# Optimization experiments

Measured on AMD Instinct MI355X. Metric: run time of the kernel, lower is better.

## Reference

```python
import jax, jax.numpy as jnp
import numpy as np

B, T = 8, 1024
C, H, K, FF, L = 512, 8, 64, 2048, 6
STATE, INP, NBINS, NACT, MAXT = 128, 128, 41, 16, 2048
EPS = 1e-5


def _ln(x, g, b):
    m = jnp.mean(x, axis=-1, keepdims=True)
    v = jnp.var(x, axis=-1, keepdims=True)
    return (x - m) / jnp.sqrt(v + EPS) * g + b


def setup_inputs() -> dict:
    key = jax.random.key(0)
    ks = jax.random.split(key, 24)
    s = 0.02
    d = {}
    d["obs"] = jax.random.normal(ks[0], (B, T, STATE), jnp.float32)
    d["action"] = jax.random.randint(ks[1], (B, T), 0, NACT)
    d["step"] = jax.random.randint(ks[2], (B, T), 0, MAXT)
    # embeddings / input projections
    d["W_obs"] = s * jax.random.normal(ks[3], (STATE, C), jnp.float32)
    d["b_obs"] = jnp.zeros((C,), jnp.float32)
    d["E_act"] = s * jax.random.normal(ks[4], (NACT, C), jnp.float32)
    d["W_traj"] = s * jax.random.normal(ks[5], (2 * C, C), jnp.float32)
    d["b_traj"] = jnp.zeros((C,), jnp.float32)
    d["E_time"] = s * jax.random.normal(ks[6], (MAXT, C), jnp.float32)
    # per-layer stacked params (scanned over leading L axis)
    d["Wq"] = s * jax.random.normal(ks[7], (L, H, C, K), jnp.float32)
    d["Wk"] = s * jax.random.normal(ks[8], (L, H, C, K), jnp.float32)
    d["Wv"] = s * jax.random.normal(ks[9], (L, H, C, K), jnp.float32)
    d["Wp"] = s * jax.random.normal(ks[10], (L, H * K, C), jnp.float32)
    d["bp"] = jnp.zeros((L, C), jnp.float32)
    d["W1"] = s * jax.random.normal(ks[11], (L, C, FF), jnp.float32)
    d["b1"] = jnp.zeros((L, FF), jnp.float32)
    d["W2"] = s * jax.random.normal(ks[12], (L, FF, C), jnp.float32)
    d["b2"] = jnp.zeros((L, C), jnp.float32)
    d["g1"] = jnp.ones((L, C), jnp.float32)
    d["be1"] = jnp.zeros((L, C), jnp.float32)
    d["g2"] = jnp.ones((L, C), jnp.float32)
    d["be2"] = jnp.zeros((L, C), jnp.float32)
    # final norm + heads
    d["gf"] = jnp.ones((C,), jnp.float32)
    d["bf"] = jnp.zeros((C,), jnp.float32)
    d["W_oh"] = s * jax.random.normal(ks[13], (C, INP), jnp.float32)
    d["b_oh"] = jnp.zeros((INP,), jnp.float32)
    d["W_rh"] = s * jax.random.normal(ks[14], (C, NBINS), jnp.float32)
    d["b_rh"] = jnp.zeros((NBINS,), jnp.float32)
    d["W_dh"] = s * jax.random.normal(ks[15], (C, 1), jnp.float32)
    d["b_dh"] = jnp.zeros((1,), jnp.float32)
    return d


def reference(obs, action, step, W_obs, b_obs, E_act, W_traj, b_traj, E_time,
              Wq, Wk, Wv, Wp, bp, W1, b1, W2, b2, g1, be1, g2, be2,
              gf, bf, W_oh, b_oh, W_rh, b_rh, W_dh, b_dh):
    Bc, Tc = obs.shape[0], obs.shape[1]
    obs_emb = obs @ W_obs + b_obs                      # [B,T,C]
    act_emb = E_act[action]                            # [B,T,C]
    token = jnp.concatenate([obs_emb, act_emb], -1) @ W_traj + b_traj
    x = token + E_time[step]                           # [B,T,C]

    causal = jnp.tril(jnp.ones((Tc, Tc), bool))        # [T,T]
    scale = 1.0 / jnp.sqrt(jnp.asarray(K, x.dtype))

    def block(x, p):
        wq, wk, wv, wp, bpl, w1, b1l, w2, b2l, ga, ba, gb, bb = p
        q = jnp.einsum('btc,hck->bhtk', x, wq)
        k = jnp.einsum('btc,hck->bhtk', x, wk)
        v = jnp.einsum('btc,hck->bhtk', x, wv)
        wei = jnp.einsum('bhtk,bhsk->bhts', q, k) * scale
        wei = jnp.where(causal, wei, -jnp.inf)
        att = jax.nn.softmax(wei, axis=-1)             # dropout off (eval)
        o = jnp.einsum('bhts,bhsk->bhtk', att, v)
        o = o.transpose(0, 2, 1, 3).reshape(Bc, Tc, H * K)  # head-wise concat
        y = o @ wp + bpl
        x = _ln(x + y, ga, ba)                         # post-norm, as in source
        y = jax.nn.relu(x @ w1 + b1l) @ w2 + b2l
        x = _ln(x + y, gb, bb)
        return x, None

    x, _ = jax.lax.scan(block, x, (Wq, Wk, Wv, Wp, bp, W1, b1, W2, b2, g1, be1, g2, be2))
    x = _ln(x, gf, bf)
    obs_logits = x @ W_oh + b_oh
    reward_logits = x @ W_rh + b_rh
    done_logits = x @ W_dh + b_dh
    return (obs_logits, reward_logits, done_logits)
```

## Files before the change

kernel.cpp:

```cpp
#include <hip/hip_runtime.h>
#include <hip/hip_bf16.h>


#define TSEQ 1024
#define BB   8
#define CDIM 512
#define HH   8
#define KHD  64
#define FFD  2048
#define LL   6
#define MROWS (BB*TSEQ)

typedef __hip_bfloat16 bf16;
typedef __attribute__((ext_vector_type(8))) short bf16x8;
typedef __attribute__((ext_vector_type(4))) short bf16x4;
typedef __attribute__((ext_vector_type(4))) float f32x4;

#define MFMA16K16(a,b,c) __builtin_amdgcn_mfma_f32_16x16x16bf16_1k(a,b,c,0,0,0)

static __device__ __forceinline__ short f2bf_bits(float x) {
    bf16 t = __float2bfloat16(x);
    return *reinterpret_cast<short*>(&t);
}
static __device__ __forceinline__ float bf2f(short b) {
    unsigned u = ((unsigned)(unsigned short)b) << 16;
    return __uint_as_float(u);
}

static __device__ __forceinline__ void gload_lds16(const bf16* g, short* l) {
    __builtin_amdgcn_global_load_lds(
        (__attribute__((address_space(1))) const void*)g,
        (__attribute__((address_space(3))) void*)l, 16, 0, 0);
}

struct PrepJob { const float* src; long dstOff; int nrows; int kd; int type; };
struct PrepArgs { PrepJob jobs[48]; };

__global__ void __launch_bounds__(256) prep_weights(PrepArgs args, bf16* __restrict__ wsb)
{
    PrepJob J = args.jobs[blockIdx.y];
    const int tilesK = (J.kd + 63) >> 6;
    const int tilesN = (J.nrows + 63) >> 6;
    const int t = blockIdx.x;
    if (t >= tilesK * tilesN) return;
    const int tn = t / tilesK, tk = t - tn * tilesK;
    const int n0 = tn << 6, k0 = tk << 6;

    __shared__ float tile[64][65];
    const int tid = threadIdx.x;
    const bool full = (J.type != 3) && (n0 + 64 <= J.nrows) && (k0 + 64 <= J.kd);

    if (full) {
        const int c4 = (tid & 15) * 4;
        const int r0 = tid >> 4;
#pragma unroll
        for (int i = 0; i < 4; ++i) {
            int kl = r0 + i * 16;
            int k = k0 + kl;
            const float* src;
            if (J.type == 0) src = J.src + (long)k * J.nrows + n0 + c4;
            else             src = J.src + ((long)(n0 >> 6) * J.kd + k) * 64 + c4;
            float4 v = *(const float4*)src;
            tile[kl][c4 + 0] = v.x; tile[kl][c4 + 1] = v.y;
            tile[kl][c4 + 2] = v.z; tile[kl][c4 + 3] = v.w;
        }
        __syncthreads();
        const int kq = (tid & 15) * 4;
        const int n1 = tid >> 4;
#pragma unroll
        for (int i = 0; i < 4; ++i) {
            int nl = n1 + i * 16;
            bf16x4 o;
#pragma unroll
            for (int j2 = 0; j2 < 4; ++j2) o[j2] = f2bf_bits(tile[kq + j2][nl]);
            *(bf16x4*)(wsb + J.dstOff + (long)(n0 + nl) * J.kd + k0 + kq) = o;
        }
    } else {
#pragma unroll
        for (int i = 0; i < 16; ++i) {
            int e = tid + i * 256;
            int kl = e >> 6, nl = e & 63;
            int k = k0 + kl, n = n0 + nl;
            float v = 0.f;
            if (J.type != 3 && k < J.kd && n < J.nrows) {
                if (J.type == 0) v = J.src[(long)k * J.nrows + n];
                else             v = J.src[((long)(n >> 6) * J.kd + k) * 64 + (n & 63)];
            }
            tile[kl][nl] = v;
        }
        __syncthreads();
#pragma unroll
        for (int i = 0; i < 16; ++i) {
            int e = tid + i * 256;
            int nl = e >> 6, kl = e & 63;
            int n = n0 + nl, k = k0 + kl;
            if (n < J.nrows && k < J.kd)
                wsb[J.dstOff + (long)n * J.kd + k] = __float2bfloat16(tile[kl][nl]);
        }
    }
}

__global__ void build_head_bias(const float* __restrict__ b_oh, const float* __restrict__ b_rh,
                                const float* __restrict__ b_dh, float* __restrict__ hb)
{
    int i = threadIdx.x;
    float v = 0.f;
    if (i < 128) v = b_oh[i];
    else if (i < 169) v = b_rh[i - 128];
    else if (i == 169) v = b_dh[0];
    hb[i] = v;
}

template<int TN, int BK, int OUTMODE, bool BIAS, bool RELU>
__global__ void __launch_bounds__(256) gemm_kernel(
    const bf16* __restrict__ A, const bf16* __restrict__ BT,
    void* __restrict__ Cout, const float* __restrict__ bias,
    int M, int N, int Kd,
    const void* __restrict__ aux1, const float* __restrict__ aux2)
{
    constexpr int NJ = TN / 32;
    constexpr int SL = BK / 8;
    constexpr int AI = (128 * BK) / (8 * 256);
    constexpr int BI = (TN  * BK) / (8 * 256);
    __shared__ short As[128 * BK];
    __shared__ short Bs[TN * BK];
    const int tid = threadIdx.x;
    const int lane = tid & 63;
    const int w = tid >> 6;
    const int wm = w >> 1, wn = w & 1;
    const int m0 = blockIdx.x * 128;
    const int n0 = blockIdx.y * TN;
    const int g = lane >> 4, lr = lane & 15;

    f32x4 acc[4][NJ] = {};

    for (int k0 = 0; k0 < Kd; k0 += BK) {
#pragma unroll
        for (int it = 0; it < AI; ++it) {
            int cbase = (w * AI + it) * 64;
            int c = cbase + lane;
            int row = c / SL, slot = c % SL;
            int ss = slot ^ (row & (SL - 1));
            gload_lds16(A + (size_t)(m0 + row) * Kd + k0 + ss * 8, As + cbase * 8);
        }
#pragma unroll
        for (int it = 0; it < BI; ++it) {
            int cbase = (w * BI + it) * 64;
            int c = cbase + lane;
            int row = c / SL, slot = c % SL;
            int ss = slot ^ (row & (SL - 1));
            gload_lds16(BT + (size_t)(n0 + row) * Kd + k0 + ss * 8, Bs + cbase * 8);
        }
        __syncthreads();
#pragma unroll
        for (int kk = 0; kk < BK; kk += 32) {
            bf16x8 af[4], bfr[NJ];
#pragma unroll
            for (int i = 0; i < 4; ++i) {
                int row = wm*64 + i*16 + lr;
                int ss = ((kk >> 3) + g) ^ (row & (SL - 1));
                af[i] = *(const bf16x8*)(As + row * BK + ss * 8);
            }
#pragma unroll
            for (int j = 0; j < NJ; ++j) {
                int row = wn*(TN/2) + j*16 + lr;
                int ss = ((kk >> 3) + g) ^ (row & (SL - 1));
                bfr[j] = *(const bf16x8*)(Bs + row * BK + ss * 8);
            }
#pragma unroll
            for (int i = 0; i < 4; ++i)
#pragma unroll
                for (int j = 0; j < NJ; ++j)
                    acc[i][j] = __builtin_amdgcn_mfma_f32_16x16x32_bf16(af[i], bfr[j], acc[i][j], 0, 0, 0);
        }
        __syncthreads();
    }

#pragma unroll
    for (int i = 0; i < 4; ++i) {
#pragma unroll
        for (int j = 0; j < NJ; ++j) {
            int col = n0 + wn*(TN/2) + j*16 + lr;
            float bv = 0.f;
            if (BIAS) bv = bias[col];
#pragma unroll
            for (int r = 0; r < 4; ++r) {
                int row = m0 + wm*64 + i*16 + g*4 + r;
                float v = acc[i][j][r] + bv;
                if (RELU) v = fmaxf(v, 0.f);
                if (OUTMODE == 1) {
                    ((bf16*)Cout)[(size_t)row * N + col] = __float2bfloat16(v);
                } else if (OUTMODE == 2) {
                    float* outf = (float*)Cout;
                    if (col < 128)      outf[(size_t)row * 128 + col] = v;
                    else if (col < 169) outf[1048576 + (size_t)row * 41 + (col - 128)] = v;
                    else if (col == 169) outf[1384448 + (size_t)row] = v;
                } else if (OUTMODE == 4) {
                    const int* stp = (const int*)aux1;
                    v += aux2[(size_t)stp[row] * 512 + col];
                    ((bf16*)Cout)[(size_t)row * N + col] = __float2bfloat16(v);
                } else {
                    ((float*)Cout)[(size_t)row * N + col] = v;
                }
            }
        }
    }
}

__global__ void __launch_bounds__(256) attn_kernel(const bf16* __restrict__ qkv, bf16* __restrict__ o)
{
    const int bh = blockIdx.x;
    const int z  = blockIdx.y;
    const int b = bh >> 3, h = bh & 7;
    const int tid = threadIdx.x, lane = tid & 63, w = tid >> 6;
    const int g = lane >> 4, lr = lane & 15;
    const int qlo = z, qhi = 15 - z;
    const float SCL = 0.125f * 1.44269504089f;

    __shared__ short Ks[128][72];
    __shared__ short Vs[8192];

    const size_t base = (size_t)b * TSEQ * 1536;

    bf16x8 qfL[2], qfH[2];
#pragma unroll
    for (int kk = 0; kk < 2; ++kk) {
        qfL[kk] = *(const bf16x8*)(qkv + base + (size_t)(qlo*64 + w*16 + lr) * 1536 + h*64 + kk*32 + g*8);
        qfH[kk] = *(const bf16x8*)(qkv + base + (size_t)(qhi*64 + w*16 + lr) * 1536 + h*64 + kk*32 + g*8);
    }

    f32x4 accL[4] = {}, accH[4] = {};
    float mL = -1e30f, lL = 0.f, mH = -1e30f, lH = 0.f;

    const short* vtr = &Vs[lane * 4];

    auto proc = [&](const bf16x8* qf, f32x4* acc, float& m, float& l, int qt, int kt) {
        f32x4 st[8];
        __builtin_amdgcn_s_setprio(1);
#pragma unroll
        for (int j = 0; j < 8; ++j) {
            st[j] = f32x4{0.f, 0.f, 0.f, 0.f};
#pragma unroll
            for (int kk = 0; kk < 2; ++kk) {
                bf16x8 af = *(const bf16x8*)(&Ks[j*16 + lr][kk*32 + g*8]);
                st[j] = __builtin_amdgcn_mfma_f32_16x16x32_bf16(af, qf[kk], st[j], 0, 0, 0);
            }
        }
        __builtin_amdgcn_s_setprio(0);
        const int qg = qt*64 + w*16 + lr;
        const bool diag = (kt == (qt >> 1));
        float vmax = -1e30f;
#pragma unroll
        for (int j = 0; j < 8; ++j)
#pragma unroll
            for (int r = 0; r < 4; ++r) {
                float v = st[j][r] * SCL;
                if (diag && (kt*128 + j*16 + g*4 + r) > qg) v = -1e30f;
                st[j][r] = v;
                vmax = fmaxf(vmax, v);
            }
        vmax = fmaxf(vmax, __shfl_xor(vmax, 16));
        vmax = fmaxf(vmax, __shfl_xor(vmax, 32));
        if (!__all(vmax <= m + 8.f)) {
            float mn = fmaxf(m, vmax);
            float alpha = exp2f(m - mn);
            l *= alpha;
            float av[4];
#pragma unroll
            for (int r = 0; r < 4; ++r) av[r] = __shfl(alpha, g*4 + r);
#pragma unroll
            for (int dj = 0; dj < 4; ++dj)
#pragma unroll
                for (int r = 0; r < 4; ++r) acc[dj][r] *= av[r];
            m = mn;
        }
        float psum = 0.f;
        bf16x4 pf[8];
#pragma unroll
        for (int j = 0; j < 8; ++j)
#pragma unroll
            for (int r = 0; r < 4; ++r) {
                float p = exp2f(st[j][r] - m);
                psum += p;
                pf[j][r] = f2bf_bits(p);
            }
        psum += __shfl_xor(psum, 16);
        psum += __shfl_xor(psum, 32);
        l += psum;
#pragma unroll
        for (int half = 0; half < 4; ++half) {
            bf16x4 vf[2][4];
#pragma unroll
            for (int jj = 0; jj < 2; ++jj)
#pragma unroll
                for (int dj = 0; dj < 4; ++dj) {
                    asm volatile("ds_read_b64_tr_b16 %0, %1"
                        : "=v"(vf[jj][dj])
                        : "v"((const __attribute__((address_space(3))) short*)
                              (vtr + ((half*2 + jj)*4 + dj) * 256)));
                }
            asm volatile("s_waitcnt lgkmcnt(0)" ::: "memory");
            __builtin_amdgcn_sched_barrier(0);
            __builtin_amdgcn_s_setprio(1);
#pragma unroll
            for (int jj = 0; jj < 2; ++jj)
#pragma unroll
                for (int dj = 0; dj < 4; ++dj)
                    acc[dj] = MFMA16K16(pf[half*2 + jj], vf[jj][dj], acc[dj]);
            __builtin_amdgcn_s_setprio(0);
        }
    };

    const int ktmax = qhi >> 1;
    for (int kt = 0; kt <= ktmax; ++kt) {
#pragma unroll
        for (int it = 0; it < 4; ++it) {
            int idx = tid + it * 256;
            int row = idx >> 3;
            int col = (idx & 7) << 3;
            *(bf16x8*)(&Ks[row][col]) =
                *(const bf16x8*)(qkv + base + (size_t)(kt*128 + row)*1536 + 512 + h*64 + col);
            bf16x8 vv = *(const bf16x8*)(qkv + base + (size_t)(kt*128 + row)*1536 + 1024 + h*64 + col);
            int dst = ((row >> 4)*4 + (col >> 4))*256 + (row & 15)*16 + (col & 8);
            *(bf16x8*)(&Vs[dst]) = vv;
        }
        __syncthreads();
        proc(qfH, accH, mH, lH, qhi, kt);
        if (kt <= (qlo >> 1)) proc(qfL, accL, mL, lL, qlo, kt);
        __syncthreads();
    }

    auto wout = [&](const f32x4* acc, float l, int qt) {
        float linv = 1.f / l;
        float lv[4];
#pragma unroll
        for (int r = 0; r < 4; ++r) lv[r] = __shfl(linv, g*4 + r);
#pragma unroll
        for (int dj = 0; dj < 4; ++dj)
#pragma unroll
            for (int r = 0; r < 4; ++r) {
                int trow = qt*64 + w*16 + g*4 + r;
                o[((size_t)(b*TSEQ + trow))*512 + h*64 + dj*16 + lr] =
                    __float2bfloat16(acc[dj][r] * lv[r]);
            }
    };
    wout(accH, lH, qhi);
    wout(accL, lL, qlo);
}

template<bool HAS_RES>
__global__ void __launch_bounds__(256) ln_kernel(
    const bf16* __restrict__ y_, const bf16* __restrict__ xin,
    bf16* __restrict__ xb,
    const float* __restrict__ gamma, const float* __restrict__ beta)
{
    int row = blockIdx.x * 4 + (threadIdx.x >> 6);
    int lane = threadIdx.x & 63;
    int c0 = lane * 8;
    size_t rb = (size_t)row * CDIM + c0;
    float u[8];
    bf16x8 yv = *(const bf16x8*)(y_ + rb);
#pragma unroll
    for (int i = 0; i < 8; ++i) u[i] = bf2f(yv[i]);
    if (HAS_RES) {
        bf16x8 xv = *(const bf16x8*)(xin + rb);
#pragma unroll
        for (int i = 0; i < 8; ++i) u[i] += bf2f(xv[i]);
    }
    float s = 0.f, sq = 0.f;
#pragma unroll
    for (int i = 0; i < 8; ++i) { s += u[i]; sq += u[i]*u[i]; }
#pragma unroll
    for (int off = 1; off < 64; off <<= 1) { s += __shfl_xor(s, off); sq += __shfl_xor(sq, off); }
    float mean = s * (1.f / 512.f);
    float var  = sq * (1.f / 512.f) - mean * mean;
    float rstd = rsqrtf(var + 1e-5f);
    float4 g0 = *(const float4*)(gamma + c0);
    float4 g1 = *(const float4*)(gamma + c0 + 4);
    float4 be0 = *(const float4*)(beta + c0);
    float4 be1v = *(const float4*)(beta + c0 + 4);
    float gv[8] = {g0.x,g0.y,g0.z,g0.w,g1.x,g1.y,g1.z,g1.w};
    float bv[8] = {be0.x,be0.y,be0.z,be0.w,be1v.x,be1v.y,be1v.z,be1v.w};
    bf16x8 ob;
#pragma unroll
    for (int i = 0; i < 8; ++i)
        ob[i] = f2bf_bits((u[i] - mean) * rstd * gv[i] + bv[i]);
    *(bf16x8*)(xb + rb) = ob;
}

__global__ void __launch_bounds__(256) obs_convert(const float* __restrict__ obs, bf16* __restrict__ out)
{
    int idx = (blockIdx.x * 256 + threadIdx.x) * 4;
    float4 v = *(const float4*)(obs + idx);
    bf16x4 o = { f2bf_bits(v.x), f2bf_bits(v.y), f2bf_bits(v.z), f2bf_bits(v.w) };
    *(bf16x4*)(out + idx) = o;
}

__global__ void __launch_bounds__(256) concat_kernel(
    const bf16* __restrict__ obs_emb, const int* __restrict__ action,
    const float* __restrict__ E_act, bf16* __restrict__ cc)
{
    int row = blockIdx.x;
    int a = action[row];
    int c = threadIdx.x * 4;
    if (c < 512) {
        *(bf16x4*)(cc + (size_t)row * 1024 + c) =
            *(const bf16x4*)(obs_emb + (size_t)row * 512 + c);
    } else {
        float4 v = *(const float4*)(E_act + (size_t)a * 512 + (c - 512));
        bf16x4 o = { f2bf_bits(v.x), f2bf_bits(v.y), f2bf_bits(v.z), f2bf_bits(v.w) };
        *(bf16x4*)(cc + (size_t)row * 1024 + c) = o;
    }
}

extern "C" void kernel_launch(void* const* d_in, const int* in_sizes, int n_in,
                              void* d_out, int out_size, void* d_ws, size_t ws_size,
                              hipStream_t stream)
{
    const float* obs    = (const float*)d_in[0];
    const int*   action = (const int*)  d_in[1];
    const int*   step   = (const int*)  d_in[2];
    const float* W_obs  = (const float*)d_in[3];
    const float* b_obs  = (const float*)d_in[4];
    const float* E_act  = (const float*)d_in[5];
    const float* W_traj = (const float*)d_in[6];
    const float* b_traj = (const float*)d_in[7];
    const float* E_time = (const float*)d_in[8];
    const float* Wq  = (const float*)d_in[9];
    const float* Wk  = (const float*)d_in[10];
    const float* Wv  = (const float*)d_in[11];
    const float* Wp  = (const float*)d_in[12];
    const float* bp  = (const float*)d_in[13];
    const float* W1  = (const float*)d_in[14];
    const float* b1  = (const float*)d_in[15];
    const float* W2  = (const float*)d_in[16];
    const float* b2  = (const float*)d_in[17];
    const float* g1  = (const float*)d_in[18];
    const float* be1 = (const float*)d_in[19];
    const float* g2  = (const float*)d_in[20];
    const float* be2 = (const float*)d_in[21];
    const float* gf  = (const float*)d_in[22];
    const float* bfp = (const float*)d_in[23];
    const float* W_oh = (const float*)d_in[24];
    const float* b_oh = (const float*)d_in[25];
    const float* W_rh = (const float*)d_in[26];
    const float* b_rh = (const float*)d_in[27];
    const float* W_dh = (const float*)d_in[28];
    const float* b_dh = (const float*)d_in[29];

    char* ws  = (char*)d_ws;
    bf16* wsb = (bf16*)ws;

    long off = 0;
    const long oWT_obs  = off; off += 512L * 128;
    const long oWT_traj = off; off += 512L * 1024;
    const long oWT_qkv  = off; off += 6L * 1536 * 512;
    const long oWT_p    = off; off += 6L * 512 * 512;
    const long oWT_1    = off; off += 6L * 2048 * 512;
    const long oWT_2    = off; off += 6L * 512 * 2048;
    const long oWT_hd   = off; off += 256L * 512;
    size_t byteOff = ((size_t)off * 2 + 255) & ~(size_t)255;

    auto take = [&](size_t bytes) {
        void* p = ws + byteOff;
        byteOff = (byteOff + bytes + 255) & ~(size_t)255;
        return p;
    };
    float* head_bias = (float*)take(256 * 4);
    bf16*  xb   = (bf16*) take((size_t)MROWS * 512 * 2);
    bf16*  qkv  = (bf16*) take((size_t)MROWS * 1536 * 2);
    bf16*  o    = (bf16*) take((size_t)MROWS * 512 * 2);
    bf16*  hbuf = (bf16*) take((size_t)MROWS * 2048 * 2);
    (void)ws_size; (void)in_sizes; (void)n_in; (void)out_size;

    PrepArgs pa;
    int nj = 0;
    auto addJob = [&](const float* src, long dstOff, int nrows, int kd, int type) {
        pa.jobs[nj].src = src; pa.jobs[nj].dstOff = dstOff;
        pa.jobs[nj].nrows = nrows; pa.jobs[nj].kd = kd; pa.jobs[nj].type = type; ++nj;
    };
    addJob(W_obs,  oWT_obs,  512, 128,  0);
    addJob(W_traj, oWT_traj, 512, 1024, 0);
    for (int l = 0; l < 6; ++l) {
        long qb = oWT_qkv + (long)l * 1536 * 512;
        addJob(Wq + (long)l * 8 * 512 * 64, qb,               512, 512, 1);
        addJob(Wk + (long)l * 8 * 512 * 64, qb + 512L * 512,  512, 512, 1);
        addJob(Wv + (long)l * 8 * 512 * 64, qb + 1024L * 512, 512, 512, 1);
        addJob(Wp + (long)l * 512 * 512,  oWT_p + (long)l * 512 * 512,  512,  512,  0);
        addJob(W1 + (long)l * 512 * 2048, oWT_1 + (long)l * 2048 * 512, 2048, 512,  0);
        addJob(W2 + (long)l * 2048 * 512, oWT_2 + (long)l * 512 * 2048, 512,  2048, 0);
    }
    addJob(W_oh, oWT_hd,             128, 512, 0);
    addJob(W_rh, oWT_hd + 128L*512,  41,  512, 0);
    addJob(W_dh, oWT_hd + 169L*512,  1,   512, 0);
    addJob(nullptr, oWT_hd + 170L*512, 86, 512, 3);

    prep_weights<<<dim3(256, nj), 256, 0, stream>>>(pa, wsb);
    build_head_bias<<<1, 256, 0, stream>>>(b_oh, b_rh, b_dh, head_bias);

    bf16* obs_bf = o;
    obs_convert<<<(MROWS * 128) / 1024, 256, 0, stream>>>(obs, obs_bf);
    bf16* obs_emb = qkv;
    gemm_kernel<64, 128, 1, true, false><<<dim3(64, 8), 256, 0, stream>>>(
        obs_bf, wsb + oWT_obs, obs_emb, b_obs, MROWS, 512, 128, nullptr, nullptr);
    bf16* cc = hbuf;
    concat_kernel<<<MROWS, 256, 0, stream>>>(obs_emb, action, E_act, cc);
    gemm_kernel<64, 128, 4, true, false><<<dim3(64, 8), 256, 0, stream>>>(
        cc, wsb + oWT_traj, xb, b_traj, MROWS, 512, 1024, step, E_time);

    for (int l = 0; l < 6; ++l) {
        gemm_kernel<128, 64, 1, false, false><<<dim3(64, 12), 256, 0, stream>>>(
            xb, wsb + oWT_qkv + (long)l * 1536 * 512, qkv, nullptr, MROWS, 1536, 512, nullptr, nullptr);
        attn_kernel<<<dim3(64, 8), 256, 0, stream>>>(qkv, o);
        gemm_kernel<64, 128, 1, true, false><<<dim3(64, 8), 256, 0, stream>>>(
            o, wsb + oWT_p + (long)l * 512 * 512, hbuf, bp + (long)l * 512, MROWS, 512, 512, nullptr, nullptr);
        ln_kernel<true><<<MROWS / 4, 256, 0, stream>>>(
            hbuf, xb, xb, g1 + l * 512, be1 + l * 512);
        gemm_kernel<128, 64, 1, true, true><<<dim3(64, 16), 256, 0, stream>>>(
            xb, wsb + oWT_1 + (long)l * 2048 * 512, hbuf, b1 + l * 2048, MROWS, 2048, 512, nullptr, nullptr);
        gemm_kernel<64, 128, 1, true, false><<<dim3(64, 8), 256, 0, stream>>>(
            hbuf, wsb + oWT_2 + (long)l * 512 * 2048, o, b2 + l * 512, MROWS, 512, 2048, nullptr, nullptr);
        ln_kernel<true><<<MROWS / 4, 256, 0, stream>>>(
            o, xb, xb, g2 + l * 512, be2 + l * 512);
    }

    ln_kernel<false><<<MROWS / 4, 256, 0, stream>>>(
        xb, nullptr, xb, gf, bfp);
    gemm_kernel<64, 128, 2, true, false><<<dim3(64, 4), 256, 0, stream>>>(
        xb, wsb + oWT_hd, d_out, head_bias, MROWS, 256, 512, nullptr, nullptr);
}
```

Measured before the change: 815.3 us.

## Add 256x256-tile 8-wave pipelined GEMM for the FFN up-projection

Adds a new GEMM kernel with 256x256 output tiles, 512 threads (8 waves), K split into 32-wide half stages, a multi-stage direct-to-LDS prefetch pipeline with explicit vmcnt waits and barriers, XOR-swizzled LDS layout, and the 16x16x32 bf16 MFMA. It replaces the 128x64-tile kernel only for the W1 (C->FF, bias+ReLU) GEMM. The goal is more data reuse per tile and better overlap of global loads with MFMA work. The cost is high register and LDS use at one block per CU, and the grid drops to 256 blocks, which may leave some CUs underused.

```diff
diff --git a/kernel.cpp b/kernel.cpp
--- a/kernel.cpp
+++ b/kernel.cpp
@@ -202,6 +202,111 @@
                 } else {
                     ((float*)Cout)[(size_t)row * N + col] = v;
                 }
+            }
+        }
+    }
+}
+
+template<bool BIAS, bool RELU>
+__global__ void __launch_bounds__(512, 1) gemm8p_kernel(
+    const bf16* __restrict__ A, const bf16* __restrict__ BT,
+    bf16* __restrict__ Cout, const float* __restrict__ bias,
+    int M, int N, int Kd)
+{
+    __shared__ short Ab[2][2][8192];
+    __shared__ short Bb[2][2][8192];
+    const int tid = threadIdx.x, lane = tid & 63, w = tid >> 6;
+    const int wr = w >> 2, wc = w & 3;
+    const int m0 = blockIdx.x * 256, n0 = blockIdx.y * 256;
+    const int g = lane >> 4, lr = lane & 15;
+
+    const int nt = Kd / 64;
+    const int NS = nt * 4;
+
+    auto stage = [&](int s) {
+        const int ts = s >> 2, kind = s & 3;
+        const int kh = kind >> 1, buf = ts & 1;
+        const bf16* src = (kind & 1) ? BT : A;
+        const int base0 = (kind & 1) ? n0 : m0;
+        short* dst = (kind & 1) ? Bb[buf][kh] : Ab[buf][kh];
+        const int k0t = ts * 64 + kh * 32;
+#pragma unroll
+        for (int it = 0; it < 2; ++it) {
+            int cbase = it * 512 + w * 64;
+            int c = cbase + lane;
+            int sr = c >> 3;
+            int u = (c & 7) ^ (sr & 7);
+            int row = sr * 2 + (u >> 2);
+            int gk = (u & 3) * 8;
+            gload_lds16(src + (size_t)(base0 + row) * Kd + k0t + gk, dst + cbase * 8);
+        }
+    };
+
+    f32x4 acc[8][4] = {};
+
+    for (int s = 0; s < 6 && s < NS; ++s) stage(s);
+    asm volatile("s_waitcnt vmcnt(8)" ::: "memory");
+    __builtin_amdgcn_s_barrier();
+    __builtin_amdgcn_sched_barrier(0);
+
+    for (int t = 0; t < nt; ++t) {
+        const int buf = t & 1;
+#pragma unroll
+        for (int q = 0; q < 4; ++q) {
+            const int kh = q >> 1;
+            const int ih = q & 1;
+            bf16x8 af[4], bfv[4];
+#pragma unroll
+            for (int i = 0; i < 4; ++i) {
+                int row = wr * 128 + (ih * 4 + i) * 16 + lr;
+                int sr = row >> 1;
+                int us = (((row & 1) * 4 + g)) ^ (sr & 7);
+                af[i] = *(const bf16x8*)(Ab[buf][kh] + sr * 64 + us * 8);
+            }
+#pragma unroll
+            for (int j = 0; j < 4; ++j) {
+                int row = wc * 64 + j * 16 + lr;
+                int sr = row >> 1;
+                int us = (((row & 1) * 4 + g)) ^ (sr & 7);
+                bfv[j] = *(const bf16x8*)(Bb[buf][kh] + sr * 64 + us * 8);
+            }
+            const int P = t * 4 + q;
+            if (P + 6 < NS) stage(P + 6);
+            if (q == 1) {
+                if (t <= nt - 2) { asm volatile("s_waitcnt vmcnt(8)" ::: "memory"); }
+                else             { asm volatile("s_waitcnt vmcnt(0)" ::: "memory"); }
+            } else if (q == 3) {
+                if (t <= nt - 3)      { asm volatile("s_waitcnt vmcnt(8)" ::: "memory"); }
+                else if (t == nt - 2) { asm volatile("s_waitcnt vmcnt(4)" ::: "memory"); }
+            }
+            __builtin_amdgcn_s_barrier();
+            __builtin_amdgcn_sched_barrier(0);
+            __builtin_amdgcn_s_setprio(1);
+#pragma unroll
+            for (int i = 0; i < 4; ++i)
+#pragma unroll
+                for (int j = 0; j < 4; ++j)
+                    acc[ih*4 + i][j] = __builtin_amdgcn_mfma_f32_16x16x32_bf16(
+                        af[i], bfv[j], acc[ih*4 + i][j], 0, 0, 0);
+            __builtin_amdgcn_s_setprio(0);
+            __builtin_amdgcn_s_barrier();
+            __builtin_amdgcn_sched_barrier(0);
+        }
+    }
+
+#pragma unroll
+    for (int i = 0; i < 8; ++i) {
+#pragma unroll
+        for (int j = 0; j < 4; ++j) {
+            int col = n0 + wc*64 + j*16 + lr;
+            float bv = 0.f;
+            if (BIAS) bv = bias[col];
+#pragma unroll
+            for (int r = 0; r < 4; ++r) {
+                int row = m0 + wr*128 + i*16 + g*4 + r;
+                float v = acc[i][j][r] + bv;
+                if (RELU) v = fmaxf(v, 0.f);
+                Cout[(size_t)row * N + col] = __float2bfloat16(v);
             }
         }
     }
@@ -516,8 +621,8 @@
             o, wsb + oWT_p + (long)l * 512 * 512, hbuf, bp + (long)l * 512, MROWS, 512, 512, nullptr, nullptr);
         ln_kernel<true><<<MROWS / 4, 256, 0, stream>>>(
             hbuf, xb, xb, g1 + l * 512, be1 + l * 512);
-        gemm_kernel<128, 64, 1, true, true><<<dim3(64, 16), 256, 0, stream>>>(
-            xb, wsb + oWT_1 + (long)l * 2048 * 512, hbuf, b1 + l * 2048, MROWS, 2048, 512, nullptr, nullptr);
+        gemm8p_kernel<true, true><<<dim3(32, 8), 512, 0, stream>>>(
+            xb, wsb + oWT_1 + (long)l * 2048 * 512, hbuf, b1 + l * 2048, MROWS, 2048, 512);
         gemm_kernel<64, 128, 1, true, false><<<dim3(64, 8), 256, 0, stream>>>(
             hbuf, wsb + oWT_2 + (long)l * 512 * 2048, o, b2 + l * 512, MROWS, 512, 2048, nullptr, nullptr);
         ln_kernel<true><<<MROWS / 4, 256, 0, stream>>>(
```

New measurement: 803.0 us. About the same (-1.5%).
